# Kernel optimization log

Measured on AMD Instinct MI355X. Metric: run time of the kernel, lower is better.

The kernel has to match this reference:

```python
import jax, jax.numpy as jnp
import numpy as np
import math

B, S, D_IN, D, H, L, NC = 4, 2048, 64, 512, 8, 2, 2
DK = D // H
FACTOR = 5
TOPK = min(FACTOR * int(math.log(S)), S)  # 35
EPS = 1e-5


def make_pe():
    # sinusoidal positional encoding [S, D]
    pos = jnp.arange(S, dtype=jnp.float32)[:, None]
    div = jnp.exp(jnp.arange(0, D, 2, dtype=jnp.float32) * (-math.log(10000.0) / D))
    pe = jnp.zeros((S, D), jnp.float32)
    pe = pe.at[:, 0::2].set(jnp.sin(pos * div)).at[:, 1::2].set(jnp.cos(pos * div))
    return pe


def layernorm(x, g, b):
    m = x.mean(-1, keepdims=True)
    v = x.var(-1, keepdims=True)
    return (x - m) / jnp.sqrt(v + EPS) * g + b


def setup_inputs() -> dict:
    key = jax.random.key(0)
    ks = iter(jax.random.split(key, 16))
    def p(shape, s=0.02):
        return jax.random.normal(next(ks), shape, jnp.float32) * s
    return dict(
        x=jax.random.normal(next(ks), (B, S, D_IN), jnp.float32),
        emb_w=p((D_IN, D)), emb_b=jnp.zeros((D,), jnp.float32),
        wq=p((L, D, D)), bq=jnp.zeros((L, D), jnp.float32),
        wk=p((L, D, D)), bk=jnp.zeros((L, D), jnp.float32),
        wv=p((L, D, D)), bv=jnp.zeros((L, D), jnp.float32),
        wo=p((L, D, D)), bo=jnp.zeros((L, D), jnp.float32),
        ff1_w=p((L, D, 4 * D)), ff1_b=jnp.zeros((L, 4 * D), jnp.float32),
        ff2_w=p((L, 4 * D, D)), ff2_b=jnp.zeros((L, D), jnp.float32),
        ln1_g=jnp.ones((L, D), jnp.float32), ln1_b=jnp.zeros((L, D), jnp.float32),
        ln2_g=jnp.ones((L, D), jnp.float32), ln2_b=jnp.zeros((L, D), jnp.float32),
        dec1_w=p((D, D // 2)), dec1_b=jnp.zeros((D // 2,), jnp.float32),
        dec2_w=p((D // 2, NC)), dec2_b=jnp.zeros((NC,), jnp.float32),
    )


def reference(x, emb_w, emb_b, wq, bq, wk, bk, wv, bv, wo, bo,
              ff1_w, ff1_b, ff2_w, ff2_b, ln1_g, ln1_b, ln2_g, ln2_b,
              dec1_w, dec1_b, dec2_w, dec2_b):
    h = x @ emb_w + emb_b + make_pe()[None]  # [B,S,D]
    scale = 1.0 / math.sqrt(DK)
    for i in range(L):
        q = (h @ wq[i] + bq[i]).reshape(B, S, H, DK).transpose(0, 2, 1, 3)
        k = (h @ wk[i] + bk[i]).reshape(B, S, H, DK).transpose(0, 2, 1, 3)
        v = (h @ wv[i] + bv[i]).reshape(B, S, H, DK).transpose(0, 2, 1, 3)
        scores = jnp.einsum('bhqd,bhkd->bhqk', q, k) * scale  # [B,H,S,S]
        top_scores, _ = jax.lax.top_k(scores, TOPK)            # [B,H,S,TOPK]
        attn = jax.nn.softmax(top_scores, axis=-1)
        # NOTE: faithful to source quirk — V sliced to its FIRST TOPK rows,
        # top_indices are discarded by the original module.
        ao = jnp.einsum('bhqk,bhkd->bhqd', attn, v[:, :, :TOPK, :])
        ao = ao.transpose(0, 2, 1, 3).reshape(B, S, D) @ wo[i] + bo[i]
        h = layernorm(h + ao, ln1_g[i], ln1_b[i])
        ff = jax.nn.relu(h @ ff1_w[i] + ff1_b[i]) @ ff2_w[i] + ff2_b[i]
        h = layernorm(h + ff, ln2_g[i], ln2_b[i])
    pooled = h.mean(axis=1)  # AdaptiveAvgPool1d(1) over seq
    out = jax.nn.relu(pooled @ dec1_w + dec1_b) @ dec2_w + dec2_b  # [B,NC]
    return out
```

## Files before the change

### kernel.cpp

```cpp
#include <hip/hip_runtime.h>
#include <cmath>

typedef unsigned short u16;
typedef __attribute__((ext_vector_type(8))) short short8;
typedef __attribute__((ext_vector_type(4))) float float4v;
typedef unsigned short ushort2v __attribute__((ext_vector_type(2)));

#define S_LEN 2048
#define NTOK  8192
#define TOPK  35
#define NT512 ((size_t)NTOK*512)

__device__ __forceinline__ u16 f2b(float f){
  unsigned int x = __float_as_uint(f);
  unsigned int r = (x + 0x7fffu + ((x >> 16) & 1u)) >> 16;
  return (u16)r;
}
__device__ __forceinline__ float b2f(u16 u){
  return __uint_as_float(((unsigned int)u) << 16);
}
__device__ __forceinline__ unsigned umax2(unsigned a, unsigned b){ return a > b ? a : b; }

__device__ __forceinline__ unsigned key_of(float f){
  unsigned u = (unsigned)f2b(f);
  unsigned m = (u & 0x8000u) ? 0xFFFFu : 0x8000u;
  return (u ^ m) & 0xFFFFu;
}
__device__ __forceinline__ float key_to_f(unsigned key){
  unsigned m = (key & 0x8000u) ? 0x8000u : 0xFFFFu;
  return __uint_as_float(((key ^ m) & 0xFFFFu) << 16);
}
__device__ __forceinline__ unsigned pkmax(unsigned a, unsigned b){
  union { unsigned u; ushort2v v; } x, y, r;
  x.u = a; y.u = b;
  r.v = __builtin_elementwise_max(x.v, y.v);
  return r.u;
}
__device__ __forceinline__ unsigned pkmin(unsigned a, unsigned b){
  union { unsigned u; ushort2v v; } x, y, r;
  x.u = a; y.u = b;
  r.v = __builtin_elementwise_min(x.v, y.v);
  return r.u;
}

__device__ __forceinline__ void gload16(const void* g, void* l){
  __builtin_amdgcn_global_load_lds(
      (const __attribute__((address_space(1))) unsigned int*)g,
      (__attribute__((address_space(3))) unsigned int*)l, 16, 0, 0);
}

struct WtArgs {
  const float* wq; const float* wk; const float* wv; const float* wo;
  const float* ff1w; const float* ff2w;
  u16* wt_qkv; u16* wt_wo; u16* wt_ff1; u16* wt_ff2;
};
__global__ void convert_all(WtArgs a){
  __shared__ u16 t[32][33];
  int l = blockIdx.y;
  int tt = blockIdx.x;
  const float* W; u16* Wt; int K, N, tx_, ty_;
  if (tt < 1024){
    int seg = tt >> 8, r = tt & 255;
    tx_ = r & 15; ty_ = r >> 4; K = 512; N = 512;
    if (seg == 0){ W = a.wq + (size_t)l*262144; Wt = a.wt_qkv + (size_t)l*786432; }
    else if (seg == 1){ W = a.wk + (size_t)l*262144; Wt = a.wt_qkv + (size_t)l*786432 + 262144; }
    else if (seg == 2){ W = a.wv + (size_t)l*262144; Wt = a.wt_qkv + (size_t)l*786432 + 524288; }
    else { W = a.wo + (size_t)l*262144; Wt = a.wt_wo + (size_t)l*262144; }
  } else if (tt < 2048){
    int r = tt - 1024;
    tx_ = r & 63; ty_ = r >> 6; K = 512; N = 2048;
    W = a.ff1w + (size_t)l*1048576; Wt = a.wt_ff1 + (size_t)l*1048576;
  } else {
    int r = tt - 2048;
    tx_ = r & 15; ty_ = r >> 4; K = 2048; N = 512;
    W = a.ff2w + (size_t)l*1048576; Wt = a.wt_ff2 + (size_t)l*1048576;
  }
  int k0 = ty_*32, n0 = tx_*32;
  int tx = threadIdx.x, ty = threadIdx.y;
  #pragma unroll
  for (int i = ty; i < 32; i += 8)
    t[i][tx] = f2b(W[(size_t)(k0+i)*N + n0+tx]);
  __syncthreads();
  #pragma unroll
  for (int i = ty; i < 32; i += 8)
    Wt[(size_t)(n0+i)*K + k0+tx] = t[tx][i];
}

__global__ void embed_kernel(const float* __restrict__ x, const float* __restrict__ w,
                             const float* __restrict__ bias, float* __restrict__ h,
                             u16* __restrict__ h16){
  int t = blockIdx.x;
  int tid = threadIdx.x;
  __shared__ float xs[64];
  if (tid < 64) xs[tid] = x[(size_t)t*64 + tid];
  __syncthreads();
  float acc0 = bias[tid];
  float acc1 = bias[tid + 256];
  #pragma unroll 8
  for (int k = 0; k < 64; ++k){
    float xv = xs[k];
    acc0 += xv * w[k*512 + tid];
    acc1 += xv * w[k*512 + tid + 256];
  }
  int s = t & (S_LEN - 1);
  const float neg_ln1e4_over_D = -9.210340371976184f / 512.f;
  int c0 = tid, c1 = tid + 256;
  float a0 = (float)s * expf((float)(c0 & ~1) * neg_ln1e4_over_D);
  float p0 = (c0 & 1) ? cosf(a0) : sinf(a0);
  float a1 = (float)s * expf((float)(c1 & ~1) * neg_ln1e4_over_D);
  float p1 = (c1 & 1) ? cosf(a1) : sinf(a1);
  float v0 = acc0 + p0, v1 = acc1 + p1;
  h[(size_t)t*512 + c0] = v0;  h16[(size_t)t*512 + c0] = f2b(v0);
  h[(size_t)t*512 + c1] = v1;  h16[(size_t)t*512 + c1] = f2b(v1);
}

template<int EPI>
__global__ __launch_bounds__(256) void gemm_mfma(
    const u16* __restrict__ A, int lda, const u16* __restrict__ Bt, int ldb,
    const float* __restrict__ bias0, const float* __restrict__ bias1,
    const float* __restrict__ bias2,
    float* __restrict__ Cf, u16* __restrict__ C16a, u16* __restrict__ C16b,
    float* __restrict__ Cv, int M, int N, int Klen){
  __shared__ __align__(16) u16 As[128*64];
  __shared__ __align__(16) u16 Bs[128*64];
  int tid = threadIdx.x;
  int w = tid >> 6, l = tid & 63, quad = l >> 4, m = l & 15;
  int m0 = blockIdx.y*128, n0 = blockIdx.x*128;
  int mh = (w >> 1)*64, nh = (w & 1)*64;
  float4v acc[4][4];
  #pragma unroll
  for (int i = 0; i < 4; ++i)
    #pragma unroll
    for (int j = 0; j < 4; ++j) acc[i][j] = (float4v){0.f,0.f,0.f,0.f};

  for (int kt = 0; kt < Klen; kt += 64){
    #pragma unroll
    for (int c = 0; c < 4; ++c){
      int g = c*256 + tid;
      int row = g >> 3, sc = g & 7, dc = sc ^ (row & 7);
      gload16(A  + (size_t)(m0+row)*lda + kt + dc*8, As + (size_t)g*8);
      gload16(Bt + (size_t)(n0+row)*ldb + kt + dc*8, Bs + (size_t)g*8);
    }
    __syncthreads();
    #pragma unroll
    for (int kk = 0; kk < 2; ++kk){
      short8 af[4], bf[4];
      #pragma unroll
      for (int i = 0; i < 4; ++i){
        int dcx = kk*4 + quad;
        int ra = mh + i*16 + m;
        af[i] = *(const short8*)(As + (size_t)(ra*8 + (dcx ^ (ra & 7)))*8);
        int rb = nh + i*16 + m;
        bf[i] = *(const short8*)(Bs + (size_t)(rb*8 + (dcx ^ (rb & 7)))*8);
      }
      #pragma unroll
      for (int i = 0; i < 4; ++i)
        #pragma unroll
        for (int j = 0; j < 4; ++j)
          acc[i][j] = __builtin_amdgcn_mfma_f32_16x16x32_bf16(af[i], bf[j], acc[i][j], 0, 0, 0);
    }
    __syncthreads();
  }

  #pragma unroll
  for (int i = 0; i < 4; ++i){
    #pragma unroll
    for (int j = 0; j < 4; ++j){
      int col = n0 + nh + j*16 + m;
      #pragma unroll
      for (int r = 0; r < 4; ++r){
        int row = m0 + mh + i*16 + quad*4 + r;
        float v = acc[i][j][r];
        if (EPI == 0){
          Cf[(size_t)row*N + col] = v + bias0[col];
        } else if (EPI == 1){
          C16a[(size_t)row*N + col] = f2b(fmaxf(v + bias0[col], 0.f));
        } else {
          int sel = col >> 9, n5 = col & 511;
          const float* bp = (sel == 0) ? bias0 : (sel == 1) ? bias1 : bias2;
          float vv = v + bp[n5];
          int d = n5 & 63, hh = n5 >> 6;
          int b = row >> 11, s = row & 2047;
          size_t idx = (((size_t)(b*8 + hh))*2048 + s)*64 + d;
          if (sel == 0)      C16a[idx] = f2b(vv);
          else if (sel == 1) C16b[idx] = f2b(vv);
          else               Cv[idx]  = vv;
        }
      }
    }
  }
}

__global__ __launch_bounds__(512) void attn_mfma_topk(
    const u16* __restrict__ qb16, const u16* __restrict__ kb16,
    const float* __restrict__ vb, u16* __restrict__ aob16){
  __shared__ unsigned pr[8*2048];
  int tid  = threadIdx.x;
  int w    = tid >> 6, l = tid & 63;
  int quad = l >> 4,  m = l & 15;
  int bh = blockIdx.y;
  int q0 = blockIdx.x * 16;

  const u16* Qp = qb16 + ((size_t)bh*2048 + q0 + m)*64 + quad*8;
  short8 a0 = *(const short8*)Qp;
  short8 a1 = *(const short8*)(Qp + 32);

  const u16* Kbase = kb16 + (size_t)bh*2048*64;
  for (int kt = 0; kt < 16; ++kt){
    int k0 = w*256 + kt*16;
    const u16* Kp = Kbase + (size_t)(k0 + m)*64 + quad*8;
    short8 b0 = *(const short8*)Kp;
    short8 b1 = *(const short8*)(Kp + 32);
    float4v acc = {0.f, 0.f, 0.f, 0.f};
    acc = __builtin_amdgcn_mfma_f32_16x16x32_bf16(a0, b0, acc, 0, 0, 0);
    acc = __builtin_amdgcn_mfma_f32_16x16x32_bf16(a1, b1, acc, 0, 0, 0);
    #pragma unroll
    for (int c = 0; c < 2; ++c){
      unsigned lo = key_of(acc[2*c]);
      unsigned hi = key_of(acc[2*c+1]);
      pr[(quad*2 + c)*2048 + k0 + m] = lo | (hi << 16);
    }
  }
  __syncthreads();

  unsigned* row = &pr[w*2048];

  unsigned sc[32];
  const uint4* p4 = (const uint4*)row;
  #pragma unroll
  for (int j = 0; j < 8; ++j){
    uint4 v4 = p4[j*64 + l];
    sc[j*4+0] = v4.x; sc[j*4+1] = v4.y; sc[j*4+2] = v4.z; sc[j*4+3] = v4.w;
  }

  #pragma unroll
  for (int k = 2; k <= 32; k <<= 1){
    #pragma unroll
    for (int j = k >> 1; j > 0; j >>= 1){
      #pragma unroll
      for (int i = 0; i < 32; ++i){
        int ixj = i ^ j;
        if (ixj > i){
          unsigned a = sc[i], b = sc[ixj];
          unsigned hi = pkmax(a, b), lo = pkmin(a, b);
          if ((i & k) == 0){ sc[i] = hi; sc[ixj] = lo; }
          else             { sc[i] = lo; sc[ixj] = hi; }
        }
      }
    }
  }

  #pragma unroll
  for (int i = 0; i < 32; ++i) row[i*64 + l] = sc[i];

  unsigned headA = sc[0] & 0xFFFFu, headB = sc[0] >> 16;
  unsigned nxtA  = sc[1] & 0xFFFFu, nxtB  = sc[1] >> 16;
  int pA = 0, pB = 0;
  unsigned tvP[TOPK];
  #pragma unroll
  for (int r = 0; r < TOPK; r += 2){
    unsigned m1 = headA | (headB << 16);
    unsigned m2 = 0;
    #pragma unroll
    for (int off = 32; off > 0; off >>= 1){
      unsigned o1 = __shfl_xor(m1, off, 64);
      unsigned o2 = __shfl_xor(m2, off, 64);
      unsigned lo = pkmin(m1, o1);
      m1 = pkmax(m1, o1);
      m2 = pkmax(pkmax(m2, o2), lo);
    }
    tvP[r] = m1;
    unsigned mA = m1 & 0xFFFFu, mB = m1 >> 16;
    int ownA = __ffsll(__ballot(headA == mA)) - 1;
    if (l == ownA){ headA = nxtA; ++pA; }
    int ownB = __ffsll(__ballot(headB == mB)) - 1;
    if (l == ownB){ headB = nxtB; ++pB; }
    nxtA = (pA + 1 < 32) ? (row[(pA + 1)*64 + l] & 0xFFFFu) : 0u;
    nxtB = (pB + 1 < 32) ? (row[(pB + 1)*64 + l] >> 16)     : 0u;
    if (r + 1 < TOPK){
      unsigned nA = (unsigned)__shfl((int)headA, ownA, 64);
      unsigned nB = (unsigned)__shfl((int)headB, ownB, 64);
      unsigned cA = umax2(m2 & 0xFFFFu, nA);
      unsigned cB = umax2(m2 >> 16, nB);
      tvP[r + 1] = cA | (cB << 16);
      int o2A = __ffsll(__ballot(headA == cA)) - 1;
      if (l == o2A){ headA = nxtA; ++pA; }
      int o2B = __ffsll(__ballot(headB == cB)) - 1;
      if (l == o2B){ headB = nxtB; ++pB; }
      nxtA = (pA + 1 < 32) ? (row[(pA + 1)*64 + l] & 0xFFFFu) : 0u;
      nxtB = (pB + 1 < 32) ? (row[(pB + 1)*64 + l] >> 16)     : 0u;
    }
  }

  const float* Vb = vb + (size_t)bh*2048*64 + l;
  float vreg[TOPK];
  #pragma unroll
  for (int r = 0; r < TOPK; ++r) vreg[r] = Vb[(size_t)r*64];
  int b = bh >> 3, hh = bh & 7;
  #pragma unroll
  for (int which = 0; which < 2; ++which){
    float tv[TOPK];
    #pragma unroll
    for (int r = 0; r < TOPK; ++r){
      unsigned key = which ? (tvP[r] >> 16) : (tvP[r] & 0xFFFFu);
      tv[r] = key_to_f(key) * 0.125f;
    }
    float mx = tv[0], denom = 0.f, acc = 0.f;
    #pragma unroll
    for (int r = 0; r < TOPK; ++r){
      float e = __expf(tv[r] - mx);
      denom += e;
      acc += e * vreg[r];
    }
    acc /= denom;
    int s = q0 + w*2 + which;
    aob16[(((size_t)(b*2048 + s))*8 + hh)*64 + l] = f2b(acc);
  }
}

__global__ void resid_ln_kernel(float* __restrict__ h, const float* __restrict__ t,
                                const float* __restrict__ g, const float* __restrict__ b,
                                u16* __restrict__ h16){
  int tok = blockIdx.x;
  int tid = threadIdx.x;
  size_t base = (size_t)tok * 512;
  float x0 = h[base + tid]       + t[base + tid];
  float x1 = h[base + tid + 256] + t[base + tid + 256];
  __shared__ float red[8];
  int wid = tid >> 6, lane = tid & 63;

  float s = x0 + x1;
  #pragma unroll
  for (int off = 32; off > 0; off >>= 1) s += __shfl_xor(s, off, 64);
  if (lane == 0) red[wid] = s;
  __syncthreads();
  float mean = (red[0] + red[1] + red[2] + red[3]) * (1.f/512.f);

  float d0 = x0 - mean, d1 = x1 - mean;
  float sq = d0*d0 + d1*d1;
  #pragma unroll
  for (int off = 32; off > 0; off >>= 1) sq += __shfl_xor(sq, off, 64);
  if (lane == 0) red[4 + wid] = sq;
  __syncthreads();
  float var = (red[4] + red[5] + red[6] + red[7]) * (1.f/512.f);
  float inv = rsqrtf(var + 1e-5f);
  float o0 = d0 * inv * g[tid]       + b[tid];
  float o1 = d1 * inv * g[tid + 256] + b[tid + 256];
  h[base + tid]         = o0;  h16[base + tid]       = f2b(o0);
  h[base + tid + 256]   = o1;  h16[base + tid + 256] = f2b(o1);
}

__global__ void pool_zero(float* __restrict__ pooled){
  pooled[blockIdx.x*512 + threadIdx.x] = 0.f;
}
__global__ void pool_kernel(const float* __restrict__ h, float* __restrict__ pooled){
  int c = blockIdx.x * 256 + threadIdx.x;
  int b = blockIdx.y;
  int s0 = blockIdx.z * 64;
  const float* p = h + ((size_t)b * 2048 + s0) * 512 + c;
  float acc = 0.f;
  #pragma unroll 8
  for (int s = 0; s < 64; ++s) acc += p[(size_t)s * 512];
  atomicAdd(&pooled[b*512 + c], acc * (1.f/2048.f));
}

__global__ void decoder_kernel(const float* __restrict__ pooled,
                               const float* __restrict__ w1, const float* __restrict__ b1,
                               const float* __restrict__ w2, const float* __restrict__ b2,
                               float* __restrict__ out){
  __shared__ float ps[4][512];
  __shared__ float hid[4][256];
  int tid = threadIdx.x;
  for (int i = tid; i < 2048; i += 256) ps[i >> 9][i & 511] = pooled[i];
  __syncthreads();
  float bb = b1[tid];
  for (int b = 0; b < 4; ++b){
    float acc = bb;
    for (int k = 0; k < 512; ++k) acc += ps[b][k] * w1[k*256 + tid];
    hid[b][tid] = fmaxf(acc, 0.f);
  }
  __syncthreads();
  if (tid < 8){
    int b = tid >> 1, c = tid & 1;
    float acc = b2[c];
    for (int j = 0; j < 256; ++j) acc += hid[b][j] * w2[j*2 + c];
    out[b*2 + c] = acc;
  }
}

extern "C" void kernel_launch(void* const* d_in, const int* in_sizes, int n_in,
                              void* d_out, int out_size, void* d_ws, size_t ws_size,
                              hipStream_t stream){
  const float* x     = (const float*)d_in[0];
  const float* emb_w = (const float*)d_in[1];
  const float* emb_b = (const float*)d_in[2];
  const float* wq    = (const float*)d_in[3];
  const float* bq    = (const float*)d_in[4];
  const float* wk    = (const float*)d_in[5];
  const float* bk    = (const float*)d_in[6];
  const float* wv    = (const float*)d_in[7];
  const float* bv    = (const float*)d_in[8];
  const float* wo    = (const float*)d_in[9];
  const float* bo    = (const float*)d_in[10];
  const float* ff1w  = (const float*)d_in[11];
  const float* ff1b  = (const float*)d_in[12];
  const float* ff2w  = (const float*)d_in[13];
  const float* ff2b  = (const float*)d_in[14];
  const float* ln1g  = (const float*)d_in[15];
  const float* ln1b  = (const float*)d_in[16];
  const float* ln2g  = (const float*)d_in[17];
  const float* ln2b  = (const float*)d_in[18];
  const float* d1w   = (const float*)d_in[19];
  const float* d1b   = (const float*)d_in[20];
  const float* d2w   = (const float*)d_in[21];
  const float* d2b   = (const float*)d_in[22];

  float* h      = (float*)d_ws;
  float* tmp    = h + NT512;
  u16*   u      = (u16*)(tmp + NT512);
  u16*   h16    = u;
  u16*   q16    = u + NT512;
  u16*   k16    = u + 2*NT512;
  float* vb     = (float*)(u + 3*NT512);
  u16*   ff16   = q16;
  u16*   aob16  = (u16*)(vb + NT512);
  u16*   wt     = aob16 + NT512;
  u16*   wt_qkv = wt;
  u16*   wt_wo  = wt_qkv + (size_t)2*1536*512;
  u16*   wt_ff1 = wt_wo  + (size_t)2*512*512;
  u16*   wt_ff2 = wt_ff1 + (size_t)2*2048*512;
  float* pooled = (float*)(wt_ff2 + (size_t)2*512*2048);

  WtArgs wa{wq, wk, wv, wo, ff1w, ff2w, wt_qkv, wt_wo, wt_ff1, wt_ff2};
  convert_all<<<dim3(3072, 2), dim3(32, 8), 0, stream>>>(wa);

  embed_kernel<<<NTOK, 256, 0, stream>>>(x, emb_w, emb_b, h, h16);

  for (int l = 0; l < 2; ++l){
    gemm_mfma<2><<<dim3(12, 64), 256, 0, stream>>>(
        h16, 512, wt_qkv + (size_t)l*1536*512, 512,
        bq + l*512, bk + l*512, bv + l*512,
        nullptr, q16, k16, vb, NTOK, 1536, 512);

    attn_mfma_topk<<<dim3(128, 32), 512, 0, stream>>>(q16, k16, vb, aob16);

    gemm_mfma<0><<<dim3(4, 64), 256, 0, stream>>>(
        aob16, 512, wt_wo + (size_t)l*512*512, 512,
        bo + l*512, nullptr, nullptr,
        tmp, nullptr, nullptr, nullptr, NTOK, 512, 512);
    resid_ln_kernel<<<NTOK, 256, 0, stream>>>(h, tmp, ln1g + l*512, ln1b + l*512, h16);

    gemm_mfma<1><<<dim3(16, 64), 256, 0, stream>>>(
        h16, 512, wt_ff1 + (size_t)l*2048*512, 512,
        ff1b + l*2048, nullptr, nullptr,
        nullptr, ff16, nullptr, nullptr, NTOK, 2048, 512);

    gemm_mfma<0><<<dim3(4, 64), 256, 0, stream>>>(
        ff16, 2048, wt_ff2 + (size_t)l*512*2048, 2048,
        ff2b + l*512, nullptr, nullptr,
        tmp, nullptr, nullptr, nullptr, NTOK, 512, 2048);
    resid_ln_kernel<<<NTOK, 256, 0, stream>>>(h, tmp, ln2g + l*512, ln2b + l*512, h16);
  }

  pool_zero<<<4, 512, 0, stream>>>(pooled);
  pool_kernel<<<dim3(2, 4, 32), 256, 0, stream>>>(h, pooled);
  decoder_kernel<<<1, 256, 0, stream>>>(pooled, d1w, d1b, d2w, d2b, (float*)d_out);
}
```

Before: 838.1 us.

## Split-K the FF2 GEMM with atomic accumulation and vectorize top-k key packing

The FF2 GEMM (K=2048) now runs as a two-way split-K over blockIdx.z, and each half adds its partial sums into the fp32 output with atomicAdd. The FF1 epilogue pre-seeds that output with the FF2 bias. The aim is to double the block count of the 256-block FF2 launch for better CU occupancy, at the cost of atomic traffic and nondeterministic summation order. In the attention kernel, the per-element bf16 sortable-key conversion is replaced by a packed bf16x2 conversion with bitwise sign flipping.

```diff
diff --git a/kernel.cpp b/kernel.cpp
--- a/kernel.cpp
+++ b/kernel.cpp
@@ -1,4 +1,5 @@
 #include <hip/hip_runtime.h>
+#include <hip/hip_bf16.h>
 #include <cmath>
 
 typedef unsigned short u16;
@@ -16,16 +17,8 @@
   unsigned int r = (x + 0x7fffu + ((x >> 16) & 1u)) >> 16;
   return (u16)r;
 }
-__device__ __forceinline__ float b2f(u16 u){
-  return __uint_as_float(((unsigned int)u) << 16);
-}
 __device__ __forceinline__ unsigned umax2(unsigned a, unsigned b){ return a > b ? a : b; }
 
-__device__ __forceinline__ unsigned key_of(float f){
-  unsigned u = (unsigned)f2b(f);
-  unsigned m = (u & 0x8000u) ? 0xFFFFu : 0x8000u;
-  return (u ^ m) & 0xFFFFu;
-}
 __device__ __forceinline__ float key_to_f(unsigned key){
   unsigned m = (key & 0x8000u) ? 0x8000u : 0xFFFFu;
   return __uint_as_float(((key ^ m) & 0xFFFFu) << 16);
@@ -127,6 +120,8 @@
   int w = tid >> 6, l = tid & 63, quad = l >> 4, m = l & 15;
   int m0 = blockIdx.y*128, n0 = blockIdx.x*128;
   int mh = (w >> 1)*64, nh = (w & 1)*64;
+  const u16* Ap  = A  + (size_t)blockIdx.z * Klen;
+  const u16* Btp = Bt + (size_t)blockIdx.z * Klen;
   float4v acc[4][4];
   #pragma unroll
   for (int i = 0; i < 4; ++i)
@@ -138,8 +133,8 @@
     for (int c = 0; c < 4; ++c){
       int g = c*256 + tid;
       int row = g >> 3, sc = g & 7, dc = sc ^ (row & 7);
-      gload16(A  + (size_t)(m0+row)*lda + kt + dc*8, As + (size_t)g*8);
-      gload16(Bt + (size_t)(n0+row)*ldb + kt + dc*8, Bs + (size_t)g*8);
+      gload16(Ap  + (size_t)(m0+row)*lda + kt + dc*8, As + (size_t)g*8);
+      gload16(Btp + (size_t)(n0+row)*ldb + kt + dc*8, Bs + (size_t)g*8);
     }
     __syncthreads();
     #pragma unroll
@@ -175,6 +170,9 @@
           Cf[(size_t)row*N + col] = v + bias0[col];
         } else if (EPI == 1){
           C16a[(size_t)row*N + col] = f2b(fmaxf(v + bias0[col], 0.f));
+          if (col < 512) Cf[(size_t)row*512 + col] = bias1[col];
+        } else if (EPI == 3){
+          atomicAdd(&Cf[(size_t)row*N + col], v);
         } else {
           int sel = col >> 9, n5 = col & 511;
           const float* bp = (sel == 0) ? bias0 : (sel == 1) ? bias1 : bias2;
@@ -216,9 +214,10 @@
     acc = __builtin_amdgcn_mfma_f32_16x16x32_bf16(a1, b1, acc, 0, 0, 0);
     #pragma unroll
     for (int c = 0; c < 2; ++c){
-      unsigned lo = key_of(acc[2*c]);
-      unsigned hi = key_of(acc[2*c+1]);
-      pr[(quad*2 + c)*2048 + k0 + m] = lo | (hi << 16);
+      union { __hip_bfloat162 b; unsigned u; } cv;
+      cv.b = __float22bfloat162_rn(float2{acc[2*c], acc[2*c+1]});
+      unsigned neg = (cv.u >> 15) & 0x00010001u;
+      pr[(quad*2 + c)*2048 + k0 + m] = cv.u ^ (0x80008000u | (neg * 0x7FFFu));
     }
   }
   __syncthreads();
@@ -452,13 +451,13 @@
 
     gemm_mfma<1><<<dim3(16, 64), 256, 0, stream>>>(
         h16, 512, wt_ff1 + (size_t)l*2048*512, 512,
-        ff1b + l*2048, nullptr, nullptr,
-        nullptr, ff16, nullptr, nullptr, NTOK, 2048, 512);
-
-    gemm_mfma<0><<<dim3(4, 64), 256, 0, stream>>>(
+        ff1b + l*2048, ff2b + l*512, nullptr,
+        tmp, ff16, nullptr, nullptr, NTOK, 2048, 512);
+
+    gemm_mfma<3><<<dim3(4, 64, 2), 256, 0, stream>>>(
         ff16, 2048, wt_ff2 + (size_t)l*512*2048, 2048,
-        ff2b + l*512, nullptr, nullptr,
-        tmp, nullptr, nullptr, nullptr, NTOK, 512, 2048);
+        nullptr, nullptr, nullptr,
+        tmp, nullptr, nullptr, nullptr, NTOK, 512, 1024);
     resid_ln_kernel<<<NTOK, 256, 0, stream>>>(h, tmp, ln2g + l*512, ln2b + l*512, h16);
   }
 
```

Measured after the change: 883.2 us. 1.05x slower.
